# Optimization experiments

Hardware: AMD Instinct MI355X
Metric: run time of the kernel (lower is better)

Reference implementation:

```python
import jax, jax.numpy as jnp
import numpy as np

N_EMBD = 1024
N_HEAD = 16
HEAD_DIM = N_EMBD // N_HEAD


def setup_inputs() -> dict:
    key = jax.random.key(0)
    ks = jax.random.split(key, 5)
    B, T = 4, 2048
    s = 0.02
    return {
        "x": jax.random.normal(ks[0], (B, T, N_EMBD), dtype=jnp.float32),
        "w_qkv": jax.random.normal(ks[1], (N_EMBD, 3 * N_EMBD), dtype=jnp.float32) * s,
        "b_qkv": jnp.zeros((3 * N_EMBD,), dtype=jnp.float32),
        "w_out": jax.random.normal(ks[2], (N_EMBD, N_EMBD), dtype=jnp.float32) * s,
        "b_out": jnp.zeros((N_EMBD,), dtype=jnp.float32),
    }


def reference(x, w_qkv, b_qkv, w_out, b_out):
    # Eval-mode forward (dropout disabled), matching the torch module's math.
    B, T, C = x.shape
    qkv = x @ w_qkv + b_qkv                      # [B,T,3C]
    q, k, v = jnp.split(qkv, 3, axis=-1)
    def heads(t):
        return t.reshape(B, T, N_HEAD, HEAD_DIM).transpose(0, 2, 1, 3)  # [B,H,T,D]
    q, k, v = heads(q), heads(k), heads(v)
    scores = jnp.einsum("bhtd,bhsd->bhts", q, k) / jnp.sqrt(jnp.float32(HEAD_DIM))
    causal = jnp.tril(jnp.ones((T, T), dtype=bool))
    scores = jnp.where(causal[None, None], scores, -jnp.inf)
    attn = jax.nn.softmax(scores, axis=-1)       # [B,H,T,T]
    y = jnp.einsum("bhts,bhsd->bhtd", attn, v)   # [B,H,T,D]
    y = y.transpose(0, 2, 1, 3).reshape(B, T, C)
    return y @ w_out + b_out
```

## Files before the change

kernel.cpp:

```cpp
#include <hip/hip_runtime.h>
#include <hip/hip_bf16.h>

#define TSEQ 2048
#define CEMB 1024

typedef __attribute__((ext_vector_type(8))) short bf16x8;
typedef __attribute__((ext_vector_type(4))) float f32x4;
typedef __attribute__((ext_vector_type(16))) float f32x16;
typedef __attribute__((ext_vector_type(4))) int i32x4;

__device__ __forceinline__ unsigned short f2bf(float f){
  return __builtin_bit_cast(unsigned short, __float2bfloat16(f));
}

__device__ __forceinline__ f32x4 MFMA16(bf16x8 a, bf16x8 b, f32x4 c){
  return __builtin_amdgcn_mfma_f32_16x16x32_bf16(a, b, c, 0, 0, 0);
}

#define GLDS(src, dst) __builtin_amdgcn_global_load_lds( \
      (const __attribute__((address_space(1))) void*)(src), \
      (__attribute__((address_space(3))) void*)(dst), 16, 0, 0)

template<int N> __device__ __forceinline__ void vmwait(){
  if constexpr (N == 0) asm volatile("s_waitcnt vmcnt(0)" ::: "memory");
  else if constexpr (N == 4) asm volatile("s_waitcnt vmcnt(4)" ::: "memory");
  else if constexpr (N == 5) asm volatile("s_waitcnt vmcnt(5)" ::: "memory");
  else if constexpr (N == 6) asm volatile("s_waitcnt vmcnt(6)" ::: "memory");
  else if constexpr (N == 7) asm volatile("s_waitcnt vmcnt(7)" ::: "memory");
  else asm volatile("s_waitcnt vmcnt(8)" ::: "memory");
}

__global__ __launch_bounds__(256) void k_prep(
    const float* __restrict__ x, unsigned short* __restrict__ xb,
    const float* __restrict__ w_qkv, unsigned short* __restrict__ wqkvT,
    const float* __restrict__ w_out, unsigned short* __restrict__ woutT)
{
  __shared__ unsigned short tile[32][33];
  const int bid = blockIdx.x, tid = threadIdx.x;
  if (bid < 8192){
    const int i = bid * 256 + tid;
    const float4 v = reinterpret_cast<const float4*>(x)[i];
    ushort4 o;
    o.x = f2bf(v.x); o.y = f2bf(v.y); o.z = f2bf(v.z); o.w = f2bf(v.w);
    reinterpret_cast<ushort4*>(xb)[i] = o;
    return;
  }
  const float* w; unsigned short* wT; int N, n0, k0;
  if (bid < 11264){
    const int b2 = bid - 8192;
    w = w_qkv; wT = wqkvT; N = 3072;
    n0 = (b2 % 96) * 32; k0 = (b2 / 96) * 32;
  } else {
    const int b3 = bid - 11264;
    w = w_out; wT = woutT; N = 1024;
    n0 = (b3 & 31) * 32; k0 = (b3 >> 5) * 32;
  }
  const int tx = tid & 31, ty = tid >> 5;
  #pragma unroll
  for (int r = 0; r < 4; ++r){
    int k = ty * 4 + r;
    tile[k][tx] = f2bf(w[(size_t)(k0 + k) * N + n0 + tx]);
  }
  __syncthreads();
  #pragma unroll
  for (int r = 0; r < 4; ++r){
    int n = ty * 4 + r;
    wT[(size_t)(n0 + n) * 1024 + k0 + tx] = tile[tx][n];
  }
}

template<bool OUT_BF16, int BM, int BN, bool FUSE_VT>
__global__ __launch_bounds__(512, 2) void k_gemm256(
    const unsigned short* __restrict__ A,
    const unsigned short* __restrict__ Bt,
    const float* __restrict__ bias,
    void* __restrict__ Cout,
    unsigned short* __restrict__ vTout,
    int M, int N, int K)
{
  constexpr int NA  = BM / 64;
  constexpr int NW  = BN / 64;
  constexpr int MM  = BM / 32;
  constexpr int MH  = MM / 2;
  constexpr int NH0 = (NW + 1) / 2;
  constexpr int NL  = NA + NW;
  constexpr int ABY = BM * 128;
  constexpr int BNB = BN * 128;
  __shared__ __align__(16) char smem[2*ABY + 2*BNB];

  const int tid = threadIdx.x;
  const int lane = tid & 63, w = tid >> 6;
  const int wm = w >> 2, wn = w & 3;
  const int l15 = lane & 15, l4 = lane >> 4;
  const int x7 = l15 & 7;

  unsigned lin = blockIdx.x;
  {
    const unsigned nwg = gridDim.x;
    const unsigned qq = nwg >> 3, rr = nwg & 7;
    const unsigned xcd = lin & 7, loc = lin >> 3;
    lin = (xcd < rr ? xcd * (qq + 1) : rr * (qq + 1) + (xcd - rr) * qq) + loc;
  }
  const unsigned ntn = (unsigned)N / BN;
  const int m0 = (int)(lin / ntn) * BM;
  const int n0 = (int)(lin % ntn) * BN;

  const int srow = lane >> 3;
  const int scx  = (lane & 7) ^ srow;
  const unsigned short* Ag = A  + (size_t)(m0 + w*8 + srow) * K + scx * 8;
  const unsigned short* Bg = Bt + (size_t)(n0 + w*8 + srow) * K + scx * 8;

  auto stageA = [&](int buf, int kt){
    const unsigned short* s = Ag + kt*64;
    char* d = smem + buf*ABY + (w << 10);
    #pragma unroll
    for (int i = 0; i < NA; ++i) GLDS(s + (size_t)(i*64)*K, d + i*8192);
  };
  auto stageB = [&](int buf, int kt){
    const unsigned short* s = Bg + kt*64;
    char* d = smem + 2*ABY + buf*BNB + (w << 10);
    #pragma unroll
    for (int i = 0; i < NW; ++i) GLDS(s + (size_t)(i*64)*K, d + i*8192);
  };

  const int arow = wm*(BM/2) + l15;
  const int brow = wn*(BN/4) + l15;
  auto rdA = [&](int buf, int m, int ks)->bf16x8 {
    return *(const bf16x8*)(smem + buf*ABY + (arow + m*16)*128 + (((ks*4 + l4) ^ x7) << 4));
  };
  auto rdB = [&](int buf, int n, int ks)->bf16x8 {
    return *(const bf16x8*)(smem + 2*ABY + buf*BNB + (brow + n*16)*128 + (((ks*4 + l4) ^ x7) << 4));
  };

  f32x4 acc[MM][NW] = {};
  const int NIT = K >> 7;

  stageA(0, 0); stageB(0, 0);
  stageA(1, 1); stageB(1, 1);
  vmwait<NL>();
  __builtin_amdgcn_s_barrier();
  asm volatile("" ::: "memory");

  for (int it = 0; it < NIT; ++it){
    const bool more = (it + 1 < NIT);
    #pragma unroll
    for (int half = 0; half < 2; ++half){
      const int buf = half;
      bf16x8 bfr[NW][2], af1[MH][2], af2[MM-MH][2];
      #pragma unroll
      for (int n = 0; n < NW; ++n){ bfr[n][0] = rdB(buf, n, 0); bfr[n][1] = rdB(buf, n, 1); }
      #pragma unroll
      for (int m = 0; m < MH; ++m){ af1[m][0] = rdA(buf, m, 0); af1[m][1] = rdA(buf, m, 1); }
      __builtin_amdgcn_s_setprio(1);
      #pragma unroll
      for (int m = 0; m < MH; ++m)
        #pragma unroll
        for (int n = 0; n < NH0; ++n)
          #pragma unroll
          for (int ks = 0; ks < 2; ++ks)
            acc[m][n] = MFMA16(af1[m][ks], bfr[n][ks], acc[m][n]);
      __builtin_amdgcn_s_setprio(0);
      #pragma unroll
      for (int m = 0; m < MM-MH; ++m){ af2[m][0] = rdA(buf, m+MH, 0); af2[m][1] = rdA(buf, m+MH, 1); }
      __builtin_amdgcn_s_setprio(1);
      #pragma unroll
      for (int m = 0; m < MH; ++m)
        #pragma unroll
        for (int n = NH0; n < NW; ++n)
          #pragma unroll
          for (int ks = 0; ks < 2; ++ks)
            acc[m][n] = MFMA16(af1[m][ks], bfr[n][ks], acc[m][n]);
      __builtin_amdgcn_s_setprio(0);
      __builtin_amdgcn_s_setprio(1);
      #pragma unroll
      for (int m = 0; m < MM-MH; ++m)
        #pragma unroll
        for (int n = NH0; n < NW; ++n)
          #pragma unroll
          for (int ks = 0; ks < 2; ++ks)
            acc[m+MH][n] = MFMA16(af2[m][ks], bfr[n][ks], acc[m+MH][n]);
      __builtin_amdgcn_s_setprio(0);
      asm volatile("s_waitcnt lgkmcnt(0)" ::: "memory");
      __builtin_amdgcn_s_barrier();
      asm volatile("" ::: "memory");
      if (more){ stageA(buf, 2*it + half + 2); stageB(buf, 2*it + half + 2); }
      __builtin_amdgcn_s_setprio(1);
      #pragma unroll
      for (int m = 0; m < MM-MH; ++m)
        #pragma unroll
        for (int n = 0; n < NH0; ++n)
          #pragma unroll
          for (int ks = 0; ks < 2; ++ks)
            acc[m+MH][n] = MFMA16(af2[m][ks], bfr[n][ks], acc[m+MH][n]);
      __builtin_amdgcn_s_setprio(0);
      if (more) vmwait<NL>();
      else      vmwait<0>();
      __builtin_amdgcn_s_barrier();
      asm volatile("" ::: "memory");
    }
  }

  float bv[NW];
  #pragma unroll
  for (int n = 0; n < NW; ++n) bv[n] = bias[n0 + wn*(BN/4) + n*16 + l15];

  #pragma unroll
  for (int m = 0; m < MM; ++m){
    const int row = m0 + wm*(BM/2) + m*16 + l4*4;
    #pragma unroll
    for (int n = 0; n < NW; ++n){
      const int colb = n0 + wn*(BN/4) + n*16;
      if (FUSE_VT && colb >= 2048){
        const int c = colb - 2048 + l15;
        const int bb = row >> 11, tt = row & 2047;
        ushort4 pk;
        pk.x = f2bf(acc[m][n][0] + bv[n]);
        pk.y = f2bf(acc[m][n][1] + bv[n]);
        pk.z = f2bf(acc[m][n][2] + bv[n]);
        pk.w = f2bf(acc[m][n][3] + bv[n]);
        *(ushort4*)&vTout[(((size_t)bb*16)*64 + c)*2048 + tt] = pk;
      } else {
        const int col = colb + l15;
        #pragma unroll
        for (int r = 0; r < 4; ++r){
          float v = acc[m][n][r] + bv[n];
          if (OUT_BF16)
            ((unsigned short*)Cout)[(size_t)(row + r) * N + col] = f2bf(v);
          else
            ((float*)Cout)[(size_t)(row + r) * N + col] = v;
        }
      }
    }
  }
}

__global__ __launch_bounds__(512, 3) void k_attn(
    const unsigned short* __restrict__ qkv,
    const unsigned short* __restrict__ vT,
    unsigned short* __restrict__ y)
{
  __shared__ __align__(16) char Ksm[2][8192];
  __shared__ __align__(16) char Vsm[2][8192];
  __shared__ float Ls[8][32];

  const int tid = threadIdx.x, lane = tid & 63, w = tid >> 6;
  const int q31 = lane & 31, hi = lane >> 5;
  const int lin = blockIdx.x;
  const int xcd = lin & 7, ii = lin >> 3;
  const int bh = xcd + ((ii & 7) << 3);
  const int p = ii >> 3;
  const int g = w >> 2, wl = w & 3;
  const int myt = g ? (15 - p) : p;
  const int b = bh >> 4, h = bh & 15;
  const size_t rowB = (size_t)b * TSEQ;

  const int wq0 = myt*128 + 32*wl, qg = wq0 + q31;
  const int nkt_my = 2*myt + 2;
  const int nktB  = 2*(15 - p) + 2;

  const float sc = 0.18033688011112042f;

  bf16x8 qf[4];
  {
    const unsigned short* qp = qkv + (rowB + qg) * 3072 + h * 64;
    #pragma unroll
    for (int c4 = 0; c4 < 4; ++c4){
      bf16x8 v = *(const bf16x8*)(qp + c4*16 + hi*8);
      #pragma unroll
      for (int j = 0; j < 8; ++j){
        const unsigned int bits = ((unsigned int)(unsigned short)v[j]) << 16;
        v[j] = (short)f2bf(__builtin_bit_cast(float, bits) * sc);
      }
      qf[c4] = v;
    }
  }

  const int kr = lane >> 3, cx = (lane & 7) ^ kr;
  const unsigned short* kgbase = qkv + (rowB + w*8 + kr) * 3072 + 1024 + h*64 + cx*8;
  const unsigned short* vgbase = vT + ((size_t)bh*64 + w*8 + kr) * 2048 + cx*8;

  #define STAGE(ktile, buf)                                                          \
    do {                                                                             \
      GLDS(kgbase + (size_t)(ktile)*64*3072, &Ksm[buf][0] + w*1024);                 \
      GLDS(vgbase + (ktile)*64,              &Vsm[buf][0] + w*1024);                 \
    } while (0)

  f32x16 O[2] = {};
  float l = 0.f;

  STAGE(0, 0);
  __syncthreads();

  int cbuf = 0;
  for (int kt = 0; kt < nktB; ++kt){
    if (kt + 1 < nktB) STAGE(kt + 1, cbuf ^ 1);

    if (kt < nkt_my){
      const char* kb = Ksm[cbuf];
      const char* vb = Vsm[cbuf];
      const bool domask = (kt*64 + 63 > wq0);
      #pragma unroll
      for (int sub = 0; sub < 2; ++sub){
        f32x16 S = {};
        __builtin_amdgcn_s_setprio(1);
        #pragma unroll
        for (int c4 = 0; c4 < 4; ++c4){
          const bf16x8 kf = *(const bf16x8*)(kb + (sub*32 + q31)*128
                                + ((((c4<<1)|hi) ^ (q31 & 7)) << 4));
          S = __builtin_amdgcn_mfma_f32_32x32x16_bf16(kf, qf[c4], S, 0, 0, 0);
        }
        __builtin_amdgcn_s_setprio(0);
        if (domask){
          #pragma unroll
          for (int r = 0; r < 16; ++r){
            const int kg = kt*64 + sub*32 + (r&3) + 8*(r>>2) + 4*hi;
            if (kg > qg) S[r] = -1e30f;
          }
        }
        float ps = 0.f;
        #pragma unroll
        for (int r = 0; r < 16; ++r){
          S[r] = __builtin_amdgcn_exp2f(S[r]);
          ps += S[r];
        }
        l += ps;
        bf16x8 paf[2];
        #pragma unroll
        for (int kc = 0; kc < 2; ++kc){
          const int e = kc * 8;
          unsigned int a, bb, cc, dd;
          asm("v_cvt_pk_bf16_f32 %0, %1, %2" : "=v"(a)  : "v"(S[e+0]), "v"(S[e+1]));
          asm("v_cvt_pk_bf16_f32 %0, %1, %2" : "=v"(bb) : "v"(S[e+4]), "v"(S[e+5]));
          asm("v_cvt_pk_bf16_f32 %0, %1, %2" : "=v"(cc) : "v"(S[e+2]), "v"(S[e+3]));
          asm("v_cvt_pk_bf16_f32 %0, %1, %2" : "=v"(dd) : "v"(S[e+6]), "v"(S[e+7]));
          asm volatile("v_permlane32_swap_b32 %0, %1" : "+v"(a),  "+v"(bb));
          asm volatile("v_permlane32_swap_b32 %0, %1" : "+v"(cc), "+v"(dd));
          i32x4 pwv; pwv[0] = (int)a; pwv[1] = (int)cc; pwv[2] = (int)bb; pwv[3] = (int)dd;
          paf[kc] = __builtin_bit_cast(bf16x8, pwv);
        }
        __builtin_amdgcn_s_setprio(1);
        #pragma unroll
        for (int kc = 0; kc < 2; ++kc){
          #pragma unroll
          for (int dblk = 0; dblk < 2; ++dblk){
            const int dr = dblk*32 + q31;
            const bf16x8 vf = *(const bf16x8*)(vb + dr*128
                                  + ((((sub<<2)|(kc<<1)|hi) ^ (dr & 7)) << 4));
            O[dblk] = __builtin_amdgcn_mfma_f32_32x32x16_bf16(paf[kc], vf, O[dblk], 0, 0, 0);
          }
        }
        __builtin_amdgcn_s_setprio(0);
      }
    }

    __syncthreads();
    cbuf ^= 1;
  }

  {
    const float lc = l + __shfl_xor(l, 32);
    if (lane < 32) Ls[w][lane] = 1.0f / lc;
  }
  __syncthreads();

  #pragma unroll
  for (int r = 0; r < 16; ++r){
    const int qloc = (r&3) + 8*(r>>2) + 4*hi;
    const float inv = Ls[w][qloc];
    const size_t row = rowB + wq0 + qloc;
    #pragma unroll
    for (int dblk = 0; dblk < 2; ++dblk)
      y[row * CEMB + h*64 + dblk*32 + q31] = f2bf(O[dblk][r] * inv);
  }
  #undef STAGE
}

extern "C" void kernel_launch(void* const* d_in, const int* in_sizes, int n_in,
                              void* d_out, int out_size, void* d_ws, size_t ws_size,
                              hipStream_t stream)
{
  const float* x     = (const float*)d_in[0];
  const float* w_qkv = (const float*)d_in[1];
  const float* b_qkv = (const float*)d_in[2];
  const float* w_out = (const float*)d_in[3];
  const float* b_out = (const float*)d_in[4];
  float* out = (float*)d_out;

  char* ws = (char*)d_ws;
  unsigned short* xb    = (unsigned short*)(ws);
  unsigned short* yb    = (unsigned short*)(ws);
  unsigned short* qkvb  = (unsigned short*)(ws + (16u<<20));
  unsigned short* vTb   = (unsigned short*)(ws + (64u<<20));
  unsigned short* wqkvT = (unsigned short*)(ws + (80u<<20));
  unsigned short* woutT = (unsigned short*)(ws + (86u<<20));

  const int M = 4 * TSEQ;

  k_prep<<<12288, 256, 0, stream>>>(x, xb, w_qkv, wqkvT, w_out, woutT);

  k_gemm256<true, 256, 192, true><<<dim3((M/256) * (3072/192)), 512, 0, stream>>>(
      xb, wqkvT, b_qkv, qkvb, vTb, M, 3072, 1024);
  k_attn<<<dim3(512), 512, 0, stream>>>(qkvb, vTb, yb);
  k_gemm256<false, 128, 128, false><<<dim3((M/128) * (1024/128)), 512, 0, stream>>>(
      yb, woutT, b_out, out, nullptr, M, 1024, 1024);
}
```

Baseline: 146.0 us.

## Restructure GEMM inner loop into per-k-slice phases with fewer live fragments

Reorganizes the GEMM main loop so each k-slice loads B fragments and half the A fragments, runs the MFMAs, then loads the other A half, instead of holding both k-slices of all fragments at once. It adds extra block barriers between phases so waves proceed in lockstep, and issues the next-tile staging only in the final phase. The aim is to cut register pressure and interleave LDS reads with MFMA work more cleanly. In exchange it adds more barriers, and it hardcodes 4 A-fragments per half, so it assumes MM == 8 (BM == 256).

```diff
diff --git a/kernel.cpp b/kernel.cpp
--- a/kernel.cpp
+++ b/kernel.cpp
@@ -81,8 +81,6 @@
   constexpr int NA  = BM / 64;
   constexpr int NW  = BN / 64;
   constexpr int MM  = BM / 32;
-  constexpr int MH  = MM / 2;
-  constexpr int NH0 = (NW + 1) / 2;
   constexpr int NL  = NA + NW;
   constexpr int ABY = BM * 128;
   constexpr int BNB = BN * 128;
@@ -146,57 +144,52 @@
     #pragma unroll
     for (int half = 0; half < 2; ++half){
       const int buf = half;
-      bf16x8 bfr[NW][2], af1[MH][2], af2[MM-MH][2];
+      bf16x8 bfr[NW], af[4];
       #pragma unroll
-      for (int n = 0; n < NW; ++n){ bfr[n][0] = rdB(buf, n, 0); bfr[n][1] = rdB(buf, n, 1); }
-      #pragma unroll
-      for (int m = 0; m < MH; ++m){ af1[m][0] = rdA(buf, m, 0); af1[m][1] = rdA(buf, m, 1); }
-      __builtin_amdgcn_s_setprio(1);
-      #pragma unroll
-      for (int m = 0; m < MH; ++m)
-        #pragma unroll
-        for (int n = 0; n < NH0; ++n)
-          #pragma unroll
-          for (int ks = 0; ks < 2; ++ks)
-            acc[m][n] = MFMA16(af1[m][ks], bfr[n][ks], acc[m][n]);
-      __builtin_amdgcn_s_setprio(0);
-      #pragma unroll
-      for (int m = 0; m < MM-MH; ++m){ af2[m][0] = rdA(buf, m+MH, 0); af2[m][1] = rdA(buf, m+MH, 1); }
-      __builtin_amdgcn_s_setprio(1);
-      #pragma unroll
-      for (int m = 0; m < MH; ++m)
-        #pragma unroll
-        for (int n = NH0; n < NW; ++n)
-          #pragma unroll
-          for (int ks = 0; ks < 2; ++ks)
-            acc[m][n] = MFMA16(af1[m][ks], bfr[n][ks], acc[m][n]);
-      __builtin_amdgcn_s_setprio(0);
-      __builtin_amdgcn_s_setprio(1);
-      #pragma unroll
-      for (int m = 0; m < MM-MH; ++m)
-        #pragma unroll
-        for (int n = NH0; n < NW; ++n)
-          #pragma unroll
-          for (int ks = 0; ks < 2; ++ks)
-            acc[m+MH][n] = MFMA16(af2[m][ks], bfr[n][ks], acc[m+MH][n]);
-      __builtin_amdgcn_s_setprio(0);
-      asm volatile("s_waitcnt lgkmcnt(0)" ::: "memory");
-      __builtin_amdgcn_s_barrier();
-      asm volatile("" ::: "memory");
-      if (more){ stageA(buf, 2*it + half + 2); stageB(buf, 2*it + half + 2); }
-      __builtin_amdgcn_s_setprio(1);
-      #pragma unroll
-      for (int m = 0; m < MM-MH; ++m)
-        #pragma unroll
-        for (int n = 0; n < NH0; ++n)
-          #pragma unroll
-          for (int ks = 0; ks < 2; ++ks)
-            acc[m+MH][n] = MFMA16(af2[m][ks], bfr[n][ks], acc[m+MH][n]);
-      __builtin_amdgcn_s_setprio(0);
-      if (more) vmwait<NL>();
-      else      vmwait<0>();
-      __builtin_amdgcn_s_barrier();
-      asm volatile("" ::: "memory");
+      for (int ks = 0; ks < 2; ++ks){
+        #pragma unroll
+        for (int n = 0; n < NW; ++n) bfr[n] = rdB(buf, n, ks);
+        #pragma unroll
+        for (int m = 0; m < 4; ++m) af[m] = rdA(buf, m, ks);
+        __builtin_amdgcn_s_barrier();
+        asm volatile("s_waitcnt lgkmcnt(0)" ::: "memory");
+        __builtin_amdgcn_s_setprio(1);
+        #pragma unroll
+        for (int m = 0; m < 4; ++m)
+          #pragma unroll
+          for (int n = 0; n < NW; ++n)
+            acc[m][n] = MFMA16(af[m], bfr[n], acc[m][n]);
+        __builtin_amdgcn_s_setprio(0);
+        __builtin_amdgcn_s_barrier();
+        #pragma unroll
+        for (int m = 0; m < 4; ++m) af[m] = rdA(buf, m + 4, ks);
+        if (ks == 0){
+          __builtin_amdgcn_s_barrier();
+          asm volatile("s_waitcnt lgkmcnt(0)" ::: "memory");
+          __builtin_amdgcn_s_setprio(1);
+          #pragma unroll
+          for (int m = 0; m < 4; ++m)
+            #pragma unroll
+            for (int n = 0; n < NW; ++n)
+              acc[m+4][n] = MFMA16(af[m], bfr[n], acc[m+4][n]);
+          __builtin_amdgcn_s_setprio(0);
+          __builtin_amdgcn_s_barrier();
+        } else {
+          asm volatile("s_waitcnt lgkmcnt(0)" ::: "memory");
+          __builtin_amdgcn_s_barrier();
+          if (more){ stageA(buf, 2*it + half + 2); stageB(buf, 2*it + half + 2); }
+          __builtin_amdgcn_s_setprio(1);
+          #pragma unroll
+          for (int m = 0; m < 4; ++m)
+            #pragma unroll
+            for (int n = 0; n < NW; ++n)
+              acc[m+4][n] = MFMA16(af[m], bfr[n], acc[m+4][n]);
+          __builtin_amdgcn_s_setprio(0);
+          if (more) vmwait<NL>();
+          else      vmwait<0>();
+          __builtin_amdgcn_s_barrier();
+        }
+      }
     }
   }
 
```

Result: slower. 149.8 us (+2.6%).

## Let idle light-tile waves help heavy tile by splitting key subtiles

Applied to the files above, without the earlier changes.

In the causal attention kernel, each block pairs a short query tile with a long one. The waves that own the short tile used to sit idle once they finished. Now they store their result, reload Q for the long tile, and take one of the two 32-key subtiles per step while the other wave group takes the other. Partial outputs and row sums are merged through shared memory at the end, and fully masked 32-key subtiles are skipped. This is meant to balance work across the 8 waves, at the cost of an extra reduction pass through LDS and more branching.

```diff
diff --git a/kernel.cpp b/kernel.cpp
--- a/kernel.cpp
+++ b/kernel.cpp
@@ -239,9 +239,9 @@
     const unsigned short* __restrict__ vT,
     unsigned short* __restrict__ y)
 {
-  __shared__ __align__(16) char Ksm[2][8192];
-  __shared__ __align__(16) char Vsm[2][8192];
+  __shared__ __align__(16) char KV[2][16384];
   __shared__ float Ls[8][32];
+  __shared__ float lB[4][32];
 
   const int tid = threadIdx.x, lane = tid & 63, w = tid >> 6;
   const int q31 = lane & 31, hi = lane >> 5;
@@ -250,19 +250,20 @@
   const int bh = xcd + ((ii & 7) << 3);
   const int p = ii >> 3;
   const int g = w >> 2, wl = w & 3;
-  const int myt = g ? (15 - p) : p;
+  const int tA = p, tB = 15 - p;
   const int b = bh >> 4, h = bh & 15;
   const size_t rowB = (size_t)b * TSEQ;
-
-  const int wq0 = myt*128 + 32*wl, qg = wq0 + q31;
-  const int nkt_my = 2*myt + 2;
-  const int nktB  = 2*(15 - p) + 2;
+  const int nktA = 2*p + 2;
+  const int nktB = 2*tB + 2;
 
   const float sc = 0.18033688011112042f;
 
+  int wq0 = (g ? tB : tA)*128 + 32*wl;
+  int qg  = wq0 + q31;
+
   bf16x8 qf[4];
-  {
-    const unsigned short* qp = qkv + (rowB + qg) * 3072 + h * 64;
+  auto loadQ = [&](int qgx){
+    const unsigned short* qp = qkv + (rowB + qgx) * 3072 + h * 64;
     #pragma unroll
     for (int c4 = 0; c4 < 4; ++c4){
       bf16x8 v = *(const bf16x8*)(qp + c4*16 + hi*8);
@@ -273,7 +274,8 @@
       }
       qf[c4] = v;
     }
-  }
+  };
+  loadQ(qg);
 
   const int kr = lane >> 3, cx = (lane & 7) ^ kr;
   const unsigned short* kgbase = qkv + (rowB + w*8 + kr) * 3072 + 1024 + h*64 + cx*8;
@@ -281,12 +283,27 @@
 
   #define STAGE(ktile, buf)                                                          \
     do {                                                                             \
-      GLDS(kgbase + (size_t)(ktile)*64*3072, &Ksm[buf][0] + w*1024);                 \
-      GLDS(vgbase + (ktile)*64,              &Vsm[buf][0] + w*1024);                 \
+      GLDS(kgbase + (size_t)(ktile)*64*3072, &KV[buf][0] + w*1024);                  \
+      GLDS(vgbase + (ktile)*64,              &KV[buf][8192] + w*1024);               \
     } while (0)
 
   f32x16 O[2] = {};
   float l = 0.f;
+
+  auto storeY = [&](int wq0s){
+    const float lc = l + __shfl_xor(l, 32);
+    if (lane < 32) Ls[w][lane] = 1.0f / lc;
+    asm volatile("s_waitcnt lgkmcnt(0)" ::: "memory");
+    #pragma unroll
+    for (int r = 0; r < 16; ++r){
+      const int qloc = (r&3) + 8*(r>>2) + 4*hi;
+      const float inv = Ls[w][qloc];
+      const size_t row = rowB + wq0s + qloc;
+      #pragma unroll
+      for (int dblk = 0; dblk < 2; ++dblk)
+        y[row * CEMB + h*64 + dblk*32 + q31] = f2bf(O[dblk][r] * inv);
+    }
+  };
 
   STAGE(0, 0);
   __syncthreads();
@@ -295,82 +312,107 @@
   for (int kt = 0; kt < nktB; ++kt){
     if (kt + 1 < nktB) STAGE(kt + 1, cbuf ^ 1);
 
-    if (kt < nkt_my){
-      const char* kb = Ksm[cbuf];
-      const char* vb = Vsm[cbuf];
-      const bool domask = (kt*64 + 63 > wq0);
-      #pragma unroll
-      for (int sub = 0; sub < 2; ++sub){
-        f32x16 S = {};
-        __builtin_amdgcn_s_setprio(1);
-        #pragma unroll
-        for (int c4 = 0; c4 < 4; ++c4){
-          const bf16x8 kf = *(const bf16x8*)(kb + (sub*32 + q31)*128
-                                + ((((c4<<1)|hi) ^ (q31 & 7)) << 4));
-          S = __builtin_amdgcn_mfma_f32_32x32x16_bf16(kf, qf[c4], S, 0, 0, 0);
+    if (!g && kt == nktA){
+      storeY(tA*128 + 32*wl);
+      #pragma unroll
+      for (int dblk = 0; dblk < 2; ++dblk) O[dblk] = (f32x16){};
+      l = 0.f;
+      wq0 = tB*128 + 32*wl;
+      qg  = wq0 + q31;
+      loadQ(qg);
+    }
+
+    const bool help = (kt >= nktA);
+    const char* kb = KV[cbuf];
+    const char* vb = KV[cbuf] + 8192;
+
+    #pragma unroll
+    for (int sub = 0; sub < 2; ++sub){
+      if (help && sub != g) continue;
+      if (kt*64 + sub*32 > wq0 + 31) continue;
+      const bool domask = (kt*64 + sub*32 + 31 > wq0);
+      f32x16 S = {};
+      __builtin_amdgcn_s_setprio(1);
+      #pragma unroll
+      for (int c4 = 0; c4 < 4; ++c4){
+        const bf16x8 kf = *(const bf16x8*)(kb + (sub*32 + q31)*128
+                              + ((((c4<<1)|hi) ^ (q31 & 7)) << 4));
+        S = __builtin_amdgcn_mfma_f32_32x32x16_bf16(kf, qf[c4], S, 0, 0, 0);
+      }
+      __builtin_amdgcn_s_setprio(0);
+      if (domask){
+        #pragma unroll
+        for (int r = 0; r < 16; ++r){
+          const int kg = kt*64 + sub*32 + (r&3) + 8*(r>>2) + 4*hi;
+          if (kg > qg) S[r] = -1e30f;
         }
-        __builtin_amdgcn_s_setprio(0);
-        if (domask){
-          #pragma unroll
-          for (int r = 0; r < 16; ++r){
-            const int kg = kt*64 + sub*32 + (r&3) + 8*(r>>2) + 4*hi;
-            if (kg > qg) S[r] = -1e30f;
-          }
+      }
+      float ps = 0.f;
+      #pragma unroll
+      for (int r = 0; r < 16; ++r){
+        S[r] = __builtin_amdgcn_exp2f(S[r]);
+        ps += S[r];
+      }
+      l += ps;
+      bf16x8 paf[2];
+      #pragma unroll
+      for (int kc = 0; kc < 2; ++kc){
+        const int e = kc * 8;
+        unsigned int a, bb, cc, dd;
+        asm("v_cvt_pk_bf16_f32 %0, %1, %2" : "=v"(a)  : "v"(S[e+0]), "v"(S[e+1]));
+        asm("v_cvt_pk_bf16_f32 %0, %1, %2" : "=v"(bb) : "v"(S[e+4]), "v"(S[e+5]));
+        asm("v_cvt_pk_bf16_f32 %0, %1, %2" : "=v"(cc) : "v"(S[e+2]), "v"(S[e+3]));
+        asm("v_cvt_pk_bf16_f32 %0, %1, %2" : "=v"(dd) : "v"(S[e+6]), "v"(S[e+7]));
+        asm volatile("v_permlane32_swap_b32 %0, %1" : "+v"(a),  "+v"(bb));
+        asm volatile("v_permlane32_swap_b32 %0, %1" : "+v"(cc), "+v"(dd));
+        i32x4 pwv; pwv[0] = (int)a; pwv[1] = (int)cc; pwv[2] = (int)bb; pwv[3] = (int)dd;
+        paf[kc] = __builtin_bit_cast(bf16x8, pwv);
+      }
+      __builtin_amdgcn_s_setprio(1);
+      #pragma unroll
+      for (int kc = 0; kc < 2; ++kc){
+        #pragma unroll
+        for (int dblk = 0; dblk < 2; ++dblk){
+          const int dr = dblk*32 + q31;
+          const bf16x8 vf = *(const bf16x8*)(vb + dr*128
+                                + ((((sub<<2)|(kc<<1)|hi) ^ (dr & 7)) << 4));
+          O[dblk] = __builtin_amdgcn_mfma_f32_32x32x16_bf16(paf[kc], vf, O[dblk], 0, 0, 0);
         }
-        float ps = 0.f;
-        #pragma unroll
-        for (int r = 0; r < 16; ++r){
-          S[r] = __builtin_amdgcn_exp2f(S[r]);
-          ps += S[r];
-        }
-        l += ps;
-        bf16x8 paf[2];
-        #pragma unroll
-        for (int kc = 0; kc < 2; ++kc){
-          const int e = kc * 8;
-          unsigned int a, bb, cc, dd;
-          asm("v_cvt_pk_bf16_f32 %0, %1, %2" : "=v"(a)  : "v"(S[e+0]), "v"(S[e+1]));
-          asm("v_cvt_pk_bf16_f32 %0, %1, %2" : "=v"(bb) : "v"(S[e+4]), "v"(S[e+5]));
-          asm("v_cvt_pk_bf16_f32 %0, %1, %2" : "=v"(cc) : "v"(S[e+2]), "v"(S[e+3]));
-          asm("v_cvt_pk_bf16_f32 %0, %1, %2" : "=v"(dd) : "v"(S[e+6]), "v"(S[e+7]));
-          asm volatile("v_permlane32_swap_b32 %0, %1" : "+v"(a),  "+v"(bb));
-          asm volatile("v_permlane32_swap_b32 %0, %1" : "+v"(cc), "+v"(dd));
-          i32x4 pwv; pwv[0] = (int)a; pwv[1] = (int)cc; pwv[2] = (int)bb; pwv[3] = (int)dd;
-          paf[kc] = __builtin_bit_cast(bf16x8, pwv);
-        }
-        __builtin_amdgcn_s_setprio(1);
-        #pragma unroll
-        for (int kc = 0; kc < 2; ++kc){
-          #pragma unroll
-          for (int dblk = 0; dblk < 2; ++dblk){
-            const int dr = dblk*32 + q31;
-            const bf16x8 vf = *(const bf16x8*)(vb + dr*128
-                                  + ((((sub<<2)|(kc<<1)|hi) ^ (dr & 7)) << 4));
-            O[dblk] = __builtin_amdgcn_mfma_f32_32x32x16_bf16(paf[kc], vf, O[dblk], 0, 0, 0);
-          }
-        }
-        __builtin_amdgcn_s_setprio(0);
-      }
+      }
+      __builtin_amdgcn_s_setprio(0);
     }
 
     __syncthreads();
     cbuf ^= 1;
   }
 
-  {
+  float* cb = (float*)&KV[0][0];
+  if (!g){
+    const int col = wl*64 + lane;
+    #pragma unroll
+    for (int dblk = 0; dblk < 2; ++dblk)
+      #pragma unroll
+      for (int r = 0; r < 16; ++r)
+        cb[(dblk*16 + r)*256 + col] = O[dblk][r];
     const float lc = l + __shfl_xor(l, 32);
+    if (lane < 32) lB[wl][lane] = lc;
+  }
+  __syncthreads();
+  if (g){
+    const int col = wl*64 + lane;
+    const float lc = l + __shfl_xor(l, 32) + lB[wl][q31];
     if (lane < 32) Ls[w][lane] = 1.0f / lc;
-  }
-  __syncthreads();
-
-  #pragma unroll
-  for (int r = 0; r < 16; ++r){
-    const int qloc = (r&3) + 8*(r>>2) + 4*hi;
-    const float inv = Ls[w][qloc];
-    const size_t row = rowB + wq0 + qloc;
-    #pragma unroll
-    for (int dblk = 0; dblk < 2; ++dblk)
-      y[row * CEMB + h*64 + dblk*32 + q31] = f2bf(O[dblk][r] * inv);
+    asm volatile("s_waitcnt lgkmcnt(0)" ::: "memory");
+    #pragma unroll
+    for (int r = 0; r < 16; ++r){
+      const int qloc = (r&3) + 8*(r>>2) + 4*hi;
+      const float inv = Ls[w][qloc];
+      const size_t row = rowB + tB*128 + 32*wl + qloc;
+      #pragma unroll
+      for (int dblk = 0; dblk < 2; ++dblk)
+        y[row * CEMB + h*64 + dblk*32 + q31] =
+            f2bf((O[dblk][r] + cb[(dblk*16 + r)*256 + col]) * inv);
+    }
   }
   #undef STAGE
 }
```

Measured after the change: 161.3 us. 1.1x slower.

## Triple-buffer K/V tiles in attention with two-ahead prefetch and partial waits

Applied to the files above, without the earlier changes.

Switches the attention kernel's K/V shared-memory staging from double to triple buffering, prefetching tile kt+2 while computing tile kt. Full __syncthreads is replaced with vmcnt(2) partial waits plus a raw s_barrier, so one tile's loads can stay in flight across the barrier. The aim is to hide global-to-LDS latency better. In exchange LDS per block grows from 32KB to 48KB, which may lower occupancy under the 3-blocks-per-CU launch bound.

```diff
diff --git a/kernel.cpp b/kernel.cpp
--- a/kernel.cpp
+++ b/kernel.cpp
@@ -23,6 +23,9 @@
 
 template<int N> __device__ __forceinline__ void vmwait(){
   if constexpr (N == 0) asm volatile("s_waitcnt vmcnt(0)" ::: "memory");
+  else if constexpr (N == 1) asm volatile("s_waitcnt vmcnt(1)" ::: "memory");
+  else if constexpr (N == 2) asm volatile("s_waitcnt vmcnt(2)" ::: "memory");
+  else if constexpr (N == 3) asm volatile("s_waitcnt vmcnt(3)" ::: "memory");
   else if constexpr (N == 4) asm volatile("s_waitcnt vmcnt(4)" ::: "memory");
   else if constexpr (N == 5) asm volatile("s_waitcnt vmcnt(5)" ::: "memory");
   else if constexpr (N == 6) asm volatile("s_waitcnt vmcnt(6)" ::: "memory");
@@ -239,8 +242,7 @@
     const unsigned short* __restrict__ vT,
     unsigned short* __restrict__ y)
 {
-  __shared__ __align__(16) char Ksm[2][8192];
-  __shared__ __align__(16) char Vsm[2][8192];
+  __shared__ __align__(16) char KV[3][16384];
   __shared__ float Ls[8][32];
 
   const int tid = threadIdx.x, lane = tid & 63, w = tid >> 6;
@@ -281,23 +283,30 @@
 
   #define STAGE(ktile, buf)                                                          \
     do {                                                                             \
-      GLDS(kgbase + (size_t)(ktile)*64*3072, &Ksm[buf][0] + w*1024);                 \
-      GLDS(vgbase + (ktile)*64,              &Vsm[buf][0] + w*1024);                 \
+      GLDS(kgbase + (size_t)(ktile)*64*3072, &KV[buf][0] + w*1024);                  \
+      GLDS(vgbase + (ktile)*64,              &KV[buf][8192] + w*1024);               \
     } while (0)
 
   f32x16 O[2] = {};
   float l = 0.f;
 
   STAGE(0, 0);
-  __syncthreads();
-
-  int cbuf = 0;
+  STAGE(1, 1);
+  vmwait<2>();
+  __builtin_amdgcn_s_barrier();
+  asm volatile("" ::: "memory");
+
+  int cur = 0;
   for (int kt = 0; kt < nktB; ++kt){
-    if (kt + 1 < nktB) STAGE(kt + 1, cbuf ^ 1);
+    const bool pre = (kt + 2 < nktB);
+    if (pre){
+      int sb = cur + 2; if (sb >= 3) sb -= 3;
+      STAGE(kt + 2, sb);
+    }
 
     if (kt < nkt_my){
-      const char* kb = Ksm[cbuf];
-      const char* vb = Vsm[cbuf];
+      const char* kb = KV[cur];
+      const char* vb = KV[cur] + 8192;
       const bool domask = (kt*64 + 63 > wq0);
       #pragma unroll
       for (int sub = 0; sub < 2; ++sub){
@@ -353,8 +362,11 @@
       }
     }
 
-    __syncthreads();
-    cbuf ^= 1;
+    if (pre) vmwait<2>();
+    else     vmwait<0>();
+    __builtin_amdgcn_s_barrier();
+    asm volatile("" ::: "memory");
+    ++cur; if (cur >= 3) cur = 0;
   }
 
   {
```

After: 148.0 us. No clear change (+1.4%).
